# Performance work log

Measured on AMD Instinct MI355X. Metric: run time of the kernel, lower is better.

## Reference

```python
import jax, jax.numpy as jnp
import numpy as np

N_NODES = 100000
N_EDGES = 3200000


def gcn_conv(x, W, b, src, dst, n_nodes):
    # x: [N, Fin] -> [N, Fout]; PyG GCNConv: linear, add self-loops,
    # symmetric norm D^-1/2 A_hat D^-1/2, sum-aggregate over incoming edges, + bias
    h = x @ W  # [N, Fout]
    loop = jnp.arange(n_nodes, dtype=src.dtype)
    src2 = jnp.concatenate([src, loop])
    dst2 = jnp.concatenate([dst, loop])
    deg = jax.ops.segment_sum(jnp.ones_like(dst2, dtype=h.dtype), dst2, num_segments=n_nodes)
    dinv = jnp.where(deg > 0, jax.lax.rsqrt(deg), 0.0)
    norm = dinv[src2] * dinv[dst2]  # [E+N]
    msgs = h[src2] * norm[:, None]  # gather + scale
    out = jax.ops.segment_sum(msgs, dst2, num_segments=n_nodes)  # scatter-add
    return out + b


def setup_inputs() -> dict:
    key = jax.random.key(0)
    k1, k2, k3, k4 = jax.random.split(key, 4)
    x = jax.random.normal(k1, (N_NODES, 16), dtype=jnp.float32)
    edge_index = jax.random.randint(k2, (2, N_EDGES), 0, N_NODES, dtype=jnp.int64)
    W1 = jax.random.normal(k3, (16, 32), dtype=jnp.float32) * (1.0 / np.sqrt(16))
    b1 = jnp.zeros((32,), dtype=jnp.float32)
    W2 = jax.random.normal(k4, (32, 3), dtype=jnp.float32) * (1.0 / np.sqrt(32))
    b2 = jnp.zeros((3,), dtype=jnp.float32)
    return {"x": x, "edge_index": edge_index, "W1": W1, "b1": b1, "W2": W2, "b2": b2}


def reference(x, edge_index, W1, b1, W2, b2):
    src, dst = edge_index[0], edge_index[1]
    n = x.shape[0]
    h = gcn_conv(x, W1, b1, src, dst, n)
    h = jax.nn.relu(h)
    h = gcn_conv(h, W2, b2, src, dst, n)
    return jax.nn.log_softmax(h, axis=1)
```

## Files before the change

kernel.cpp:

```cpp
#include <hip/hip_runtime.h>
#include <math.h>


#define NN 100000
#define NE 3200000
#define BSH 7
#define NPB 128
#define NB  ((NN + NPB - 1) / NPB)
#define EPB 12544
#define CAP 6144
#define SCAP 5632

__device__ __forceinline__ float bl(unsigned u) { return __uint_as_float(u << 16); }
__device__ __forceinline__ float bh(unsigned u) { return __uint_as_float(u & 0xFFFF0000u); }
__device__ __forceinline__ unsigned rne(float f) {
    unsigned u = __float_as_uint(f);
    return (u + 0x7FFFu + ((u >> 16) & 1u)) >> 16;
}

typedef int vint4 __attribute__((ext_vector_type(4)));
typedef float floatx2 __attribute__((ext_vector_type(2)));

#define FP8SCALE 8.0f
#define FP8INV   0.125f


__global__ void __launch_bounds__(256) k_zero(int* __restrict__ bcur) {
    int t = blockIdx.x * 256 + threadIdx.x;
    if (t < NB) bcur[t] = 0;
}

__global__ void __launch_bounds__(1024) k_partition(
        const int* __restrict__ src, const int* __restrict__ dst,
        int* __restrict__ bcur, unsigned int* __restrict__ ebuf, int E) {
    __shared__ int hist[NB];
    __shared__ int lbase[NB];
    __shared__ int gbase[NB];
    __shared__ int lcur[NB];
    __shared__ unsigned int sebuf[EPB];
    __shared__ unsigned short sbkt[EPB];
    __shared__ int wsum[16];
    int tid = threadIdx.x;
    int e0 = blockIdx.x * EPB;
    int e1 = min(e0 + EPB, E);
    int cnt = e1 - e0;
    int cnt4 = cnt >> 2;
    if (tid < NB) { hist[tid] = 0; lcur[tid] = 0; }
    __syncthreads();
    const vint4* d4 = (const vint4*)(dst + e0);
    vint4 dc[4];
#pragma unroll
    for (int r = 0; r < 4; r++) {
        int i4 = r * 1024 + tid;
        if (i4 < cnt4) {
            dc[r] = d4[i4];
            atomicAdd(&hist[dc[r].x >> BSH], 1);
            atomicAdd(&hist[dc[r].y >> BSH], 1);
            atomicAdd(&hist[dc[r].z >> BSH], 1);
            atomicAdd(&hist[dc[r].w >> BSH], 1);
        }
    }
    __syncthreads();
    int lane = tid & 63, w = tid >> 6;
    {
        int v = (tid < NB) ? hist[tid] : 0;
        int incl = v;
#pragma unroll
        for (int off = 1; off < 64; off <<= 1) {
            int u = __shfl_up(incl, off);
            if (lane >= off) incl += u;
        }
        if (lane == 63) wsum[w] = incl;
        __syncthreads();
        int woff = 0;
#pragma unroll
        for (int k = 0; k < 16; k++) woff += (k < w) ? wsum[k] : 0;
        int excl = incl - v + woff;
        if (tid < NB) {
            lbase[tid] = excl;
            gbase[tid] = tid * CAP + (v ? atomicAdd(&bcur[tid], v) : 0);
        }
        __syncthreads();
    }
    const vint4* s4 = (const vint4*)(src + e0);
#pragma unroll
    for (int r = 0; r < 4; r++) {
        int i4 = r * 1024 + tid;
        if (i4 < cnt4) {
            vint4 sv = s4[i4];
            int d, b, p;
            d = dc[r].x; b = d >> BSH; p = lbase[b] + atomicAdd(&lcur[b], 1);
            sebuf[p] = (unsigned)sv.x | ((unsigned)(d & (NPB - 1)) << 20);
            sbkt[p] = (unsigned short)b;
            d = dc[r].y; b = d >> BSH; p = lbase[b] + atomicAdd(&lcur[b], 1);
            sebuf[p] = (unsigned)sv.y | ((unsigned)(d & (NPB - 1)) << 20);
            sbkt[p] = (unsigned short)b;
            d = dc[r].z; b = d >> BSH; p = lbase[b] + atomicAdd(&lcur[b], 1);
            sebuf[p] = (unsigned)sv.z | ((unsigned)(d & (NPB - 1)) << 20);
            sbkt[p] = (unsigned short)b;
            d = dc[r].w; b = d >> BSH; p = lbase[b] + atomicAdd(&lcur[b], 1);
            sebuf[p] = (unsigned)sv.w | ((unsigned)(d & (NPB - 1)) << 20);
            sbkt[p] = (unsigned short)b;
        }
    }
    __syncthreads();
    for (int p = tid; p < cnt; p += 1024) {
        int b = sbkt[p];
        ebuf[gbase[b] + (p - lbase[b])] = sebuf[p];
    }
}

__global__ void __launch_bounds__(256) k_B(
        const unsigned int* __restrict__ ebuf, const int* __restrict__ bcur,
        const float* __restrict__ x, int* __restrict__ deg,
        unsigned int* __restrict__ xsb, int N) {
    __shared__ int hist[NPB];
    int b = blockIdx.x, tid = threadIdx.x;
    int beg = b * CAP, cnt = bcur[b];
    int cnt4 = cnt >> 2;
    if (tid < NPB) hist[tid] = 0;
    __syncthreads();
    const uint4* e4 = (const uint4*)(ebuf + beg);
    for (int j4 = tid; j4 < cnt4; j4 += 256) {
        uint4 pv = e4[j4];
        atomicAdd(&hist[pv.x >> 20], 1);
        atomicAdd(&hist[pv.y >> 20], 1);
        atomicAdd(&hist[pv.z >> 20], 1);
        atomicAdd(&hist[pv.w >> 20], 1);
    }
    for (int j = (cnt4 << 2) + tid; j < cnt; j += 256)
        atomicAdd(&hist[ebuf[beg + j] >> 20], 1);
    __syncthreads();
    if (tid < NPB) {
        int node = b * NPB + tid;
        if (node < N) {
            int v = hist[tid];
            deg[node] = v;
            float di = rsqrtf((float)(v + 1));
            float s = di * FP8SCALE;
            const float4* x4 = (const float4*)(x + (size_t)node * 16);
            float4 A = x4[0], Bv = x4[1], Cv = x4[2], Dv = x4[3];
            unsigned d0, d1, d2, d3;
            d0 = __builtin_amdgcn_cvt_pk_fp8_f32(A.x * s, A.y * s, 0, false);
            d0 = __builtin_amdgcn_cvt_pk_fp8_f32(A.z * s, A.w * s, d0, true);
            d1 = __builtin_amdgcn_cvt_pk_fp8_f32(Bv.x * s, Bv.y * s, 0, false);
            d1 = __builtin_amdgcn_cvt_pk_fp8_f32(Bv.z * s, Bv.w * s, d1, true);
            d2 = __builtin_amdgcn_cvt_pk_fp8_f32(Cv.x * s, Cv.y * s, 0, false);
            d2 = __builtin_amdgcn_cvt_pk_fp8_f32(Cv.z * s, Cv.w * s, d2, true);
            d3 = __builtin_amdgcn_cvt_pk_fp8_f32(Dv.x * s, Dv.y * s, 0, false);
            d3 = __builtin_amdgcn_cvt_pk_fp8_f32(Dv.z * s, Dv.w * s, d3, true);
            uint4 o; o.x = d0; o.y = d1; o.z = d2; o.w = d3;
            ((uint4*)xsb)[node] = o;
        }
    }
}

__global__ void __launch_bounds__(512) k_L1(
        const unsigned int* __restrict__ ebuf, const int* __restrict__ bcur,
        const int* __restrict__ deg, const unsigned int* __restrict__ xsb,
        const float* __restrict__ W1, const float* __restrict__ b1,
        const float* __restrict__ W2, unsigned int* __restrict__ g2b, int N) {
    __shared__ int scol[SCAP];
    __shared__ float sacc[NPB][17];
    __shared__ int sdeg[NPB];
    __shared__ int base[NPB];
    __shared__ int lcur[NPB];
    __shared__ float sdinv[NPB];
    __shared__ float W1s[512];
    __shared__ float W2s[96];
    __shared__ float b1s[32];
    __shared__ int wsum[2];
    int b = blockIdx.x, tid = threadIdx.x;
    int beg = b * CAP;
    int cnt = bcur[b];
    int cl = min(cnt, SCAP);
    int cl4 = cl >> 2;
    W1s[tid] = W1[tid];
    if (tid < 96) W2s[tid] = W2[tid];
    if (tid < 32) b1s[tid] = b1[tid];
    int lane = tid & 63, w = tid >> 6;
    int v = 0;
    if (tid < NPB) {
        int node = b * NPB + tid;
        v = (node < N) ? deg[node] : 0;
        sdeg[tid] = v;
        lcur[tid] = 0;
        sdinv[tid] = rsqrtf((float)(v + 1));
    }
    int incl = v;
#pragma unroll
    for (int off = 1; off < 64; off <<= 1) {
        int u = __shfl_up(incl, off);
        if (lane >= off) incl += u;
    }
    if (tid < NPB && lane == 63) wsum[w] = incl;
    __syncthreads();
    if (tid < NPB) base[tid] = incl - v + ((w == 1) ? wsum[0] : 0);
    __syncthreads();
    const uint4* e4 = (const uint4*)(ebuf + beg);
    for (int j4 = tid; j4 < cl4; j4 += 512) {
        uint4 pv = e4[j4];
        int dl, pos;
        dl = (int)(pv.x >> 20); pos = base[dl] + atomicAdd(&lcur[dl], 1);
        if (pos < SCAP) scol[pos] = (int)(pv.x & 0xFFFFF);
        dl = (int)(pv.y >> 20); pos = base[dl] + atomicAdd(&lcur[dl], 1);
        if (pos < SCAP) scol[pos] = (int)(pv.y & 0xFFFFF);
        dl = (int)(pv.z >> 20); pos = base[dl] + atomicAdd(&lcur[dl], 1);
        if (pos < SCAP) scol[pos] = (int)(pv.z & 0xFFFFF);
        dl = (int)(pv.w >> 20); pos = base[dl] + atomicAdd(&lcur[dl], 1);
        if (pos < SCAP) scol[pos] = (int)(pv.w & 0xFFFFF);
    }
    for (int j = (cl4 << 2) + tid; j < cl; j += 512) {
        unsigned pe = ebuf[beg + j];
        int dl = (int)(pe >> 20);
        int pos = base[dl] + atomicAdd(&lcur[dl], 1);
        if (pos < SCAP) scol[pos] = (int)(pe & 0xFFFFF);
    }
    __syncthreads();
    {
        int lo = tid & 7;
        int nb8 = tid >> 3;
        const uint4* xb = (const uint4*)xsb;
        float a0 = 0.f, a1 = 0.f, a2 = 0.f, a3 = 0.f;
        float a4 = 0.f, a5 = 0.f, a6 = 0.f, a7 = 0.f;
        float a8 = 0.f, a9 = 0.f, a10 = 0.f, a11 = 0.f;
        float a12 = 0.f, a13 = 0.f, a14 = 0.f, a15 = 0.f;
#pragma unroll
        for (int p = 0; p < 2; p++) {
            int nib = p * 64 + nb8;
            int jb = base[nib];
            int je = jb + sdeg[nib];
            a0 = a1 = a2 = a3 = a4 = a5 = a6 = a7 = 0.f;
            a8 = a9 = a10 = a11 = a12 = a13 = a14 = a15 = 0.f;
            int j = jb + lo;
            while (j + 8 < je) {
                int s0 = scol[j], s1 = scol[j + 8];
                uint4 q0 = xb[s0];
                uint4 q1 = xb[s1];
                floatx2 f;
                f = __builtin_amdgcn_cvt_pk_f32_fp8(q0.x, false); a0 += f.x; a1 += f.y;
                f = __builtin_amdgcn_cvt_pk_f32_fp8(q0.x, true);  a2 += f.x; a3 += f.y;
                f = __builtin_amdgcn_cvt_pk_f32_fp8(q0.y, false); a4 += f.x; a5 += f.y;
                f = __builtin_amdgcn_cvt_pk_f32_fp8(q0.y, true);  a6 += f.x; a7 += f.y;
                f = __builtin_amdgcn_cvt_pk_f32_fp8(q0.z, false); a8 += f.x; a9 += f.y;
                f = __builtin_amdgcn_cvt_pk_f32_fp8(q0.z, true);  a10 += f.x; a11 += f.y;
                f = __builtin_amdgcn_cvt_pk_f32_fp8(q0.w, false); a12 += f.x; a13 += f.y;
                f = __builtin_amdgcn_cvt_pk_f32_fp8(q0.w, true);  a14 += f.x; a15 += f.y;
                f = __builtin_amdgcn_cvt_pk_f32_fp8(q1.x, false); a0 += f.x; a1 += f.y;
                f = __builtin_amdgcn_cvt_pk_f32_fp8(q1.x, true);  a2 += f.x; a3 += f.y;
                f = __builtin_amdgcn_cvt_pk_f32_fp8(q1.y, false); a4 += f.x; a5 += f.y;
                f = __builtin_amdgcn_cvt_pk_f32_fp8(q1.y, true);  a6 += f.x; a7 += f.y;
                f = __builtin_amdgcn_cvt_pk_f32_fp8(q1.z, false); a8 += f.x; a9 += f.y;
                f = __builtin_amdgcn_cvt_pk_f32_fp8(q1.z, true);  a10 += f.x; a11 += f.y;
                f = __builtin_amdgcn_cvt_pk_f32_fp8(q1.w, false); a12 += f.x; a13 += f.y;
                f = __builtin_amdgcn_cvt_pk_f32_fp8(q1.w, true);  a14 += f.x; a15 += f.y;
                j += 16;
            }
            if (j < je) {
                int s = scol[j];
                uint4 qq = xb[s];
                floatx2 f;
                f = __builtin_amdgcn_cvt_pk_f32_fp8(qq.x, false); a0 += f.x; a1 += f.y;
                f = __builtin_amdgcn_cvt_pk_f32_fp8(qq.x, true);  a2 += f.x; a3 += f.y;
                f = __builtin_amdgcn_cvt_pk_f32_fp8(qq.y, false); a4 += f.x; a5 += f.y;
                f = __builtin_amdgcn_cvt_pk_f32_fp8(qq.y, true);  a6 += f.x; a7 += f.y;
                f = __builtin_amdgcn_cvt_pk_f32_fp8(qq.z, false); a8 += f.x; a9 += f.y;
                f = __builtin_amdgcn_cvt_pk_f32_fp8(qq.z, true);  a10 += f.x; a11 += f.y;
                f = __builtin_amdgcn_cvt_pk_f32_fp8(qq.w, false); a12 += f.x; a13 += f.y;
                f = __builtin_amdgcn_cvt_pk_f32_fp8(qq.w, true);  a14 += f.x; a15 += f.y;
            }
#pragma unroll
            for (int off = 4; off >= 1; off >>= 1) {
                a0 += __shfl_down(a0, off);   a1 += __shfl_down(a1, off);
                a2 += __shfl_down(a2, off);   a3 += __shfl_down(a3, off);
                a4 += __shfl_down(a4, off);   a5 += __shfl_down(a5, off);
                a6 += __shfl_down(a6, off);   a7 += __shfl_down(a7, off);
                a8 += __shfl_down(a8, off);   a9 += __shfl_down(a9, off);
                a10 += __shfl_down(a10, off); a11 += __shfl_down(a11, off);
                a12 += __shfl_down(a12, off); a13 += __shfl_down(a13, off);
                a14 += __shfl_down(a14, off); a15 += __shfl_down(a15, off);
            }
            if (lo == 0) {
                sacc[nib][0] = a0;   sacc[nib][1] = a1;
                sacc[nib][2] = a2;   sacc[nib][3] = a3;
                sacc[nib][4] = a4;   sacc[nib][5] = a5;
                sacc[nib][6] = a6;   sacc[nib][7] = a7;
                sacc[nib][8] = a8;   sacc[nib][9] = a9;
                sacc[nib][10] = a10; sacc[nib][11] = a11;
                sacc[nib][12] = a12; sacc[nib][13] = a13;
                sacc[nib][14] = a14; sacc[nib][15] = a15;
            }
        }
    }
    __syncthreads();
    if (tid < NPB) {
        int node = b * NPB + tid;
        if (node < N) {
            float di = sdinv[tid];
            const uint4* xb = (const uint4*)xsb;
            uint4 sq = xb[node];
            floatx2 e0 = __builtin_amdgcn_cvt_pk_f32_fp8(sq.x, false);
            floatx2 e1 = __builtin_amdgcn_cvt_pk_f32_fp8(sq.x, true);
            floatx2 e2 = __builtin_amdgcn_cvt_pk_f32_fp8(sq.y, false);
            floatx2 e3 = __builtin_amdgcn_cvt_pk_f32_fp8(sq.y, true);
            floatx2 e4v = __builtin_amdgcn_cvt_pk_f32_fp8(sq.z, false);
            floatx2 e5 = __builtin_amdgcn_cvt_pk_f32_fp8(sq.z, true);
            floatx2 e6 = __builtin_amdgcn_cvt_pk_f32_fp8(sq.w, false);
            floatx2 e7 = __builtin_amdgcn_cvt_pk_f32_fp8(sq.w, true);
            float a[16] = {
                (sacc[tid][0] + e0.x) * FP8INV,  (sacc[tid][1] + e0.y) * FP8INV,
                (sacc[tid][2] + e1.x) * FP8INV,  (sacc[tid][3] + e1.y) * FP8INV,
                (sacc[tid][4] + e2.x) * FP8INV,  (sacc[tid][5] + e2.y) * FP8INV,
                (sacc[tid][6] + e3.x) * FP8INV,  (sacc[tid][7] + e3.y) * FP8INV,
                (sacc[tid][8] + e4v.x) * FP8INV, (sacc[tid][9] + e4v.y) * FP8INV,
                (sacc[tid][10] + e5.x) * FP8INV, (sacc[tid][11] + e5.y) * FP8INV,
                (sacc[tid][12] + e6.x) * FP8INV, (sacc[tid][13] + e6.y) * FP8INV,
                (sacc[tid][14] + e7.x) * FP8INV, (sacc[tid][15] + e7.y) * FP8INV};
            float p0 = 0.f, p1 = 0.f, p2 = 0.f;
#pragma unroll
            for (int jj = 0; jj < 32; jj++) {
                float o = 0.f;
#pragma unroll
                for (int k = 0; k < 16; k++) o = fmaf(a[k], W1s[k * 32 + jj], o);
                float z = fmaxf(fmaf(di, o, b1s[jj]), 0.f);
                p0 = fmaf(z, W2s[jj * 3 + 0], p0);
                p1 = fmaf(z, W2s[jj * 3 + 1], p1);
                p2 = fmaf(z, W2s[jj * 3 + 2], p2);
            }
            uint2 o;
            o.x = rne(p0 * di) | (rne(p1 * di) << 16);
            o.y = rne(p2 * di);
            ((uint2*)g2b)[node] = o;
        }
    }
}

__global__ void __launch_bounds__(512) k_L2(
        const unsigned int* __restrict__ ebuf, const int* __restrict__ bcur,
        const int* __restrict__ deg, const unsigned int* __restrict__ g2b,
        const float* __restrict__ b2, float* __restrict__ out, int N) {
    __shared__ int scol[SCAP];
    __shared__ int sdeg[NPB];
    __shared__ int base[NPB];
    __shared__ int lcur[NPB];
    __shared__ float sdinv[NPB];
    __shared__ int wsum[2];
    int b = blockIdx.x, tid = threadIdx.x;
    int beg = b * CAP;
    int cnt = bcur[b];
    int cl = min(cnt, SCAP);
    int cl4 = cl >> 2;
    int lane = tid & 63, w = tid >> 6;
    int v = 0;
    if (tid < NPB) {
        int node = b * NPB + tid;
        v = (node < N) ? deg[node] : 0;
        sdeg[tid] = v;
        lcur[tid] = 0;
        sdinv[tid] = rsqrtf((float)(v + 1));
    }
    int incl = v;
#pragma unroll
    for (int off = 1; off < 64; off <<= 1) {
        int u = __shfl_up(incl, off);
        if (lane >= off) incl += u;
    }
    if (tid < NPB && lane == 63) wsum[w] = incl;
    __syncthreads();
    if (tid < NPB) base[tid] = incl - v + ((w == 1) ? wsum[0] : 0);
    __syncthreads();
    const uint4* e4 = (const uint4*)(ebuf + beg);
    for (int j4 = tid; j4 < cl4; j4 += 512) {
        uint4 pv = e4[j4];
        int dl, pos;
        dl = (int)(pv.x >> 20); pos = base[dl] + atomicAdd(&lcur[dl], 1);
        if (pos < SCAP) scol[pos] = (int)(pv.x & 0xFFFFF);
        dl = (int)(pv.y >> 20); pos = base[dl] + atomicAdd(&lcur[dl], 1);
        if (pos < SCAP) scol[pos] = (int)(pv.y & 0xFFFFF);
        dl = (int)(pv.z >> 20); pos = base[dl] + atomicAdd(&lcur[dl], 1);
        if (pos < SCAP) scol[pos] = (int)(pv.z & 0xFFFFF);
        dl = (int)(pv.w >> 20); pos = base[dl] + atomicAdd(&lcur[dl], 1);
        if (pos < SCAP) scol[pos] = (int)(pv.w & 0xFFFFF);
    }
    for (int j = (cl4 << 2) + tid; j < cl; j += 512) {
        unsigned pe = ebuf[beg + j];
        int dl = (int)(pe >> 20);
        int pos = base[dl] + atomicAdd(&lcur[dl], 1);
        if (pos < SCAP) scol[pos] = (int)(pe & 0xFFFFF);
    }
    __syncthreads();
    {
        int lo = tid & 7;
        const uint2* gb = (const uint2*)g2b;
#pragma unroll
        for (int p = 0; p < 2; p++) {
            int nib = p * 64 + (tid >> 3);
            int node = b * NPB + nib;
            int jb = base[nib];
            int je = jb + sdeg[nib];
            float a0 = 0.f, a1 = 0.f, a2 = 0.f;
            int j = jb + lo;
            while (j + 8 < je) {
                uint2 v0 = gb[scol[j]];
                uint2 v1 = gb[scol[j + 8]];
                a0 += bl(v0.x); a1 += bh(v0.x); a2 += bl(v0.y);
                a0 += bl(v1.x); a1 += bh(v1.x); a2 += bl(v1.y);
                j += 16;
            }
            if (j < je) {
                uint2 vv = gb[scol[j]];
                a0 += bl(vv.x); a1 += bh(vv.x); a2 += bl(vv.y);
            }
#pragma unroll
            for (int off = 4; off >= 1; off >>= 1) {
                a0 += __shfl_down(a0, off);
                a1 += __shfl_down(a1, off);
                a2 += __shfl_down(a2, off);
            }
            if (lo == 0 && node < N) {
                float di = sdinv[nib];
                uint2 sv = gb[node];
                float v0 = fmaf(di, a0 + bl(sv.x), b2[0]);
                float v1 = fmaf(di, a1 + bh(sv.x), b2[1]);
                float v2 = fmaf(di, a2 + bl(sv.y), b2[2]);
                float m = fmaxf(v0, fmaxf(v1, v2));
                float lse = m + logf(expf(v0 - m) + expf(v1 - m) + expf(v2 - m));
                out[(size_t)node * 3 + 0] = v0 - lse;
                out[(size_t)node * 3 + 1] = v1 - lse;
                out[(size_t)node * 3 + 2] = v2 - lse;
            }
        }
    }
}


extern "C" void kernel_launch(void* const* d_in, const int* in_sizes, int n_in,
                              void* d_out, int out_size, void* d_ws, size_t ws_size,
                              hipStream_t stream) {
    const float* x  = (const float*)d_in[0];
    const int*   ei = (const int*)d_in[1];
    const float* W1 = (const float*)d_in[2];
    const float* b1 = (const float*)d_in[3];
    const float* W2 = (const float*)d_in[4];
    const float* b2 = (const float*)d_in[5];
    float* out = (float*)d_out;

    const int* src = ei;
    const int* dst = ei + NE;

    unsigned int* ebuf = (unsigned int*)d_ws;
    unsigned int* xsb  = ebuf + (size_t)NB * CAP;
    unsigned int* g2b  = xsb + (size_t)NN * 4;
    int*          deg  = (int*)(g2b + (size_t)NN * 2);
    int*          bcur = deg + NN;

    const int B = 256;
    int gbP = (NE + EPB - 1) / EPB;
    int gbZ = (NB + B - 1) / B;

    k_zero<<<gbZ, B, 0, stream>>>(bcur);
    k_partition<<<gbP, 1024, 0, stream>>>(src, dst, bcur, ebuf, NE);
    k_B<<<NB, B, 0, stream>>>(ebuf, bcur, x, deg, xsb, NN);
    k_L1<<<NB, 512, 0, stream>>>(ebuf, bcur, deg, xsb, W1, b1, W2, g2b, NN);
    k_L2<<<NB, 512, 0, stream>>>(ebuf, bcur, deg, g2b, b2, out, NN);
}
```

Baseline: 81.54 us.

## Build per-bucket CSR column list once in degree kernel and reuse in both layers

The degree kernel now also computes per-bucket prefix offsets and counting-sorts the edge sources by destination into shared memory, then writes the sorted column list to a new global buffer. Both aggregation kernels now copy that pre-sorted list straight into shared memory instead of redoing the atomic counting sort. This removes one redundant shared-atomic sort pass in exchange for an extra global write and read of the column array, plus a larger block for the degree kernel.

Measured after the change: 83.81 us. 2.8% more time.

```diff
diff --git a/kernel.cpp b/kernel.cpp
--- a/kernel.cpp
+++ b/kernel.cpp
@@ -110,31 +110,46 @@
     }
 }
 
-__global__ void __launch_bounds__(256) k_B(
+__global__ void __launch_bounds__(512) k_BS(
         const unsigned int* __restrict__ ebuf, const int* __restrict__ bcur,
         const float* __restrict__ x, int* __restrict__ deg,
-        unsigned int* __restrict__ xsb, int N) {
+        unsigned int* __restrict__ xsb, int* __restrict__ colg, int N) {
+    __shared__ unsigned int se[SCAP];
     __shared__ int hist[NPB];
+    __shared__ int base[NPB];
+    __shared__ int lcur[NPB];
+    __shared__ int wsum[2];
     int b = blockIdx.x, tid = threadIdx.x;
     int beg = b * CAP, cnt = bcur[b];
-    int cnt4 = cnt >> 2;
-    if (tid < NPB) hist[tid] = 0;
+    int cl = min(cnt, SCAP);
+    int cl4 = cl >> 2;
+    if (tid < NPB) { hist[tid] = 0; lcur[tid] = 0; }
     __syncthreads();
     const uint4* e4 = (const uint4*)(ebuf + beg);
-    for (int j4 = tid; j4 < cnt4; j4 += 256) {
+    for (int j4 = tid; j4 < cl4; j4 += 512) {
         uint4 pv = e4[j4];
         atomicAdd(&hist[pv.x >> 20], 1);
         atomicAdd(&hist[pv.y >> 20], 1);
         atomicAdd(&hist[pv.z >> 20], 1);
         atomicAdd(&hist[pv.w >> 20], 1);
     }
-    for (int j = (cnt4 << 2) + tid; j < cnt; j += 256)
+    for (int j = (cl4 << 2) + tid; j < cnt; j += 512)
         atomicAdd(&hist[ebuf[beg + j] >> 20], 1);
     __syncthreads();
+    int lane = tid & 63, w = tid >> 6;
+    int v = (tid < NPB) ? hist[tid] : 0;
+    int incl = v;
+#pragma unroll
+    for (int off = 1; off < 64; off <<= 1) {
+        int u = __shfl_up(incl, off);
+        if (lane >= off) incl += u;
+    }
+    if (tid < NPB && lane == 63) wsum[w] = incl;
+    __syncthreads();
+    if (tid < NPB) base[tid] = incl - v + ((w == 1) ? wsum[0] : 0);
     if (tid < NPB) {
         int node = b * NPB + tid;
         if (node < N) {
-            int v = hist[tid];
             deg[node] = v;
             float di = rsqrtf((float)(v + 1));
             float s = di * FP8SCALE;
@@ -153,10 +168,34 @@
             ((uint4*)xsb)[node] = o;
         }
     }
+    __syncthreads();
+    for (int j4 = tid; j4 < cl4; j4 += 512) {
+        uint4 pv = e4[j4];
+        int dl, pos;
+        dl = (int)(pv.x >> 20); pos = base[dl] + atomicAdd(&lcur[dl], 1);
+        if (pos < SCAP) se[pos] = pv.x & 0xFFFFF;
+        dl = (int)(pv.y >> 20); pos = base[dl] + atomicAdd(&lcur[dl], 1);
+        if (pos < SCAP) se[pos] = pv.y & 0xFFFFF;
+        dl = (int)(pv.z >> 20); pos = base[dl] + atomicAdd(&lcur[dl], 1);
+        if (pos < SCAP) se[pos] = pv.z & 0xFFFFF;
+        dl = (int)(pv.w >> 20); pos = base[dl] + atomicAdd(&lcur[dl], 1);
+        if (pos < SCAP) se[pos] = pv.w & 0xFFFFF;
+    }
+    for (int j = (cl4 << 2) + tid; j < cl; j += 512) {
+        unsigned pe = ebuf[beg + j];
+        int dl = (int)(pe >> 20);
+        int pos = base[dl] + atomicAdd(&lcur[dl], 1);
+        if (pos < SCAP) se[pos] = pe & 0xFFFFF;
+    }
+    __syncthreads();
+    uint4* cg4 = (uint4*)(colg + beg);
+    const uint4* se4 = (const uint4*)se;
+    for (int j4 = tid; j4 < cl4; j4 += 512) cg4[j4] = se4[j4];
+    for (int j = (cl4 << 2) + tid; j < cl; j += 512) colg[beg + j] = (int)se[j];
 }
 
 __global__ void __launch_bounds__(512) k_L1(
-        const unsigned int* __restrict__ ebuf, const int* __restrict__ bcur,
+        const int* __restrict__ colg, const int* __restrict__ bcur,
         const int* __restrict__ deg, const unsigned int* __restrict__ xsb,
         const float* __restrict__ W1, const float* __restrict__ b1,
         const float* __restrict__ W2, unsigned int* __restrict__ g2b, int N) {
@@ -164,7 +203,6 @@
     __shared__ float sacc[NPB][17];
     __shared__ int sdeg[NPB];
     __shared__ int base[NPB];
-    __shared__ int lcur[NPB];
     __shared__ float sdinv[NPB];
     __shared__ float W1s[512];
     __shared__ float W2s[96];
@@ -172,8 +210,7 @@
     __shared__ int wsum[2];
     int b = blockIdx.x, tid = threadIdx.x;
     int beg = b * CAP;
-    int cnt = bcur[b];
-    int cl = min(cnt, SCAP);
+    int cl = min(bcur[b], SCAP);
     int cl4 = cl >> 2;
     W1s[tid] = W1[tid];
     if (tid < 96) W2s[tid] = W2[tid];
@@ -184,7 +221,6 @@
         int node = b * NPB + tid;
         v = (node < N) ? deg[node] : 0;
         sdeg[tid] = v;
-        lcur[tid] = 0;
         sdinv[tid] = rsqrtf((float)(v + 1));
     }
     int incl = v;
@@ -196,35 +232,19 @@
     if (tid < NPB && lane == 63) wsum[w] = incl;
     __syncthreads();
     if (tid < NPB) base[tid] = incl - v + ((w == 1) ? wsum[0] : 0);
-    __syncthreads();
-    const uint4* e4 = (const uint4*)(ebuf + beg);
-    for (int j4 = tid; j4 < cl4; j4 += 512) {
-        uint4 pv = e4[j4];
-        int dl, pos;
-        dl = (int)(pv.x >> 20); pos = base[dl] + atomicAdd(&lcur[dl], 1);
-        if (pos < SCAP) scol[pos] = (int)(pv.x & 0xFFFFF);
-        dl = (int)(pv.y >> 20); pos = base[dl] + atomicAdd(&lcur[dl], 1);
-        if (pos < SCAP) scol[pos] = (int)(pv.y & 0xFFFFF);
-        dl = (int)(pv.z >> 20); pos = base[dl] + atomicAdd(&lcur[dl], 1);
-        if (pos < SCAP) scol[pos] = (int)(pv.z & 0xFFFFF);
-        dl = (int)(pv.w >> 20); pos = base[dl] + atomicAdd(&lcur[dl], 1);
-        if (pos < SCAP) scol[pos] = (int)(pv.w & 0xFFFFF);
-    }
-    for (int j = (cl4 << 2) + tid; j < cl; j += 512) {
-        unsigned pe = ebuf[beg + j];
-        int dl = (int)(pe >> 20);
-        int pos = base[dl] + atomicAdd(&lcur[dl], 1);
-        if (pos < SCAP) scol[pos] = (int)(pe & 0xFFFFF);
+    {
+        const uint4* cg4 = (const uint4*)(colg + beg);
+        uint4* sc4 = (uint4*)scol;
+        for (int j4 = tid; j4 < cl4; j4 += 512) sc4[j4] = cg4[j4];
+        for (int j = (cl4 << 2) + tid; j < cl; j += 512) scol[j] = colg[beg + j];
     }
     __syncthreads();
     {
         int lo = tid & 7;
         int nb8 = tid >> 3;
         const uint4* xb = (const uint4*)xsb;
-        float a0 = 0.f, a1 = 0.f, a2 = 0.f, a3 = 0.f;
-        float a4 = 0.f, a5 = 0.f, a6 = 0.f, a7 = 0.f;
-        float a8 = 0.f, a9 = 0.f, a10 = 0.f, a11 = 0.f;
-        float a12 = 0.f, a13 = 0.f, a14 = 0.f, a15 = 0.f;
+        float a0, a1, a2, a3, a4, a5, a6, a7;
+        float a8, a9, a10, a11, a12, a13, a14, a15;
 #pragma unroll
         for (int p = 0; p < 2; p++) {
             int nib = p * 64 + nb8;
@@ -336,19 +356,17 @@
 }
 
 __global__ void __launch_bounds__(512) k_L2(
-        const unsigned int* __restrict__ ebuf, const int* __restrict__ bcur,
+        const int* __restrict__ colg, const int* __restrict__ bcur,
         const int* __restrict__ deg, const unsigned int* __restrict__ g2b,
         const float* __restrict__ b2, float* __restrict__ out, int N) {
     __shared__ int scol[SCAP];
     __shared__ int sdeg[NPB];
     __shared__ int base[NPB];
-    __shared__ int lcur[NPB];
     __shared__ float sdinv[NPB];
     __shared__ int wsum[2];
     int b = blockIdx.x, tid = threadIdx.x;
     int beg = b * CAP;
-    int cnt = bcur[b];
-    int cl = min(cnt, SCAP);
+    int cl = min(bcur[b], SCAP);
     int cl4 = cl >> 2;
     int lane = tid & 63, w = tid >> 6;
     int v = 0;
@@ -356,7 +374,6 @@
         int node = b * NPB + tid;
         v = (node < N) ? deg[node] : 0;
         sdeg[tid] = v;
-        lcur[tid] = 0;
         sdinv[tid] = rsqrtf((float)(v + 1));
     }
     int incl = v;
@@ -368,25 +385,11 @@
     if (tid < NPB && lane == 63) wsum[w] = incl;
     __syncthreads();
     if (tid < NPB) base[tid] = incl - v + ((w == 1) ? wsum[0] : 0);
-    __syncthreads();
-    const uint4* e4 = (const uint4*)(ebuf + beg);
-    for (int j4 = tid; j4 < cl4; j4 += 512) {
-        uint4 pv = e4[j4];
-        int dl, pos;
-        dl = (int)(pv.x >> 20); pos = base[dl] + atomicAdd(&lcur[dl], 1);
-        if (pos < SCAP) scol[pos] = (int)(pv.x & 0xFFFFF);
-        dl = (int)(pv.y >> 20); pos = base[dl] + atomicAdd(&lcur[dl], 1);
-        if (pos < SCAP) scol[pos] = (int)(pv.y & 0xFFFFF);
-        dl = (int)(pv.z >> 20); pos = base[dl] + atomicAdd(&lcur[dl], 1);
-        if (pos < SCAP) scol[pos] = (int)(pv.z & 0xFFFFF);
-        dl = (int)(pv.w >> 20); pos = base[dl] + atomicAdd(&lcur[dl], 1);
-        if (pos < SCAP) scol[pos] = (int)(pv.w & 0xFFFFF);
-    }
-    for (int j = (cl4 << 2) + tid; j < cl; j += 512) {
-        unsigned pe = ebuf[beg + j];
-        int dl = (int)(pe >> 20);
-        int pos = base[dl] + atomicAdd(&lcur[dl], 1);
-        if (pos < SCAP) scol[pos] = (int)(pe & 0xFFFFF);
+    {
+        const uint4* cg4 = (const uint4*)(colg + beg);
+        uint4* sc4 = (uint4*)scol;
+        for (int j4 = tid; j4 < cl4; j4 += 512) sc4[j4] = cg4[j4];
+        for (int j = (cl4 << 2) + tid; j < cl; j += 512) scol[j] = colg[beg + j];
     }
     __syncthreads();
     {
@@ -449,7 +452,8 @@
     const int* dst = ei + NE;
 
     unsigned int* ebuf = (unsigned int*)d_ws;
-    unsigned int* xsb  = ebuf + (size_t)NB * CAP;
+    int*          colg = (int*)(ebuf + (size_t)NB * CAP);
+    unsigned int* xsb  = (unsigned int*)(colg + (size_t)NB * CAP);
     unsigned int* g2b  = xsb + (size_t)NN * 4;
     int*          deg  = (int*)(g2b + (size_t)NN * 2);
     int*          bcur = deg + NN;
@@ -460,7 +464,7 @@
 
     k_zero<<<gbZ, B, 0, stream>>>(bcur);
     k_partition<<<gbP, 1024, 0, stream>>>(src, dst, bcur, ebuf, NE);
-    k_B<<<NB, B, 0, stream>>>(ebuf, bcur, x, deg, xsb, NN);
-    k_L1<<<NB, 512, 0, stream>>>(ebuf, bcur, deg, xsb, W1, b1, W2, g2b, NN);
-    k_L2<<<NB, 512, 0, stream>>>(ebuf, bcur, deg, g2b, b2, out, NN);
-}
+    k_BS<<<NB, 512, 0, stream>>>(ebuf, bcur, x, deg, xsb, colg, NN);
+    k_L1<<<NB, 512, 0, stream>>>(colg, bcur, deg, xsb, W1, b1, W2, g2b, NN);
+    k_L2<<<NB, 512, 0, stream>>>(colg, bcur, deg, g2b, b2, out, NN);
+}
```
